# Performance work log

Measured on AMD Instinct MI355X. Metric: run time of the kernel, lower is better.

The kernel has to match this reference:

```python
import jax, jax.numpy as jnp
import numpy as np

N, D, K = 65536, 512, 512


def _l2norm(x, eps=1e-12):
    # matches torch F.normalize: x / max(||x||, eps)
    n = jnp.linalg.norm(x, axis=-1, keepdims=True)
    return x / jnp.maximum(n, eps)


def setup_inputs() -> dict:
    key = jax.random.key(0)
    k1, k2 = jax.random.split(key)
    return {
        "embeddings": jax.random.normal(k1, (N, D), dtype=jnp.float32),
        "labels": jax.random.randint(k2, (N,), 0, K),
        "w": jnp.asarray(10.0, dtype=jnp.float32),
        "b": jnp.asarray(-5.0, dtype=jnp.float32),
        "num_classes": K,
    }


def reference(embeddings, labels, w, b, num_classes):
    # assumes labels take all values in [0, num_classes) so torch.unique's
    # inverse == labels (holds for the generated inputs: 65536 draws over 512 ids)
    labels = labels.astype(jnp.int32)
    n = embeddings.shape[0]
    emb = _l2norm(embeddings)                                        # [N, D]
    ones = jnp.ones((n,), dtype=emb.dtype)
    counts = jax.ops.segment_sum(ones, labels, num_segments=num_classes)   # [K]
    sums = jax.ops.segment_sum(emb, labels, num_segments=num_classes)      # [K, D]
    centroids = sums / jnp.maximum(counts, 1.0)[:, None]             # [K, D] (NOT re-normalized, per source)
    sims = emb @ centroids.T                                          # [N, K]
    # exclusive centroid for each sample's own class, vectorized over N
    cnt_i = counts[labels]                                            # [N]
    denom = jnp.maximum(cnt_i - 1.0, 1.0)[:, None]
    excl = _l2norm((sums[labels] - emb) / denom)                      # [N, D]
    own = jnp.sum(emb * excl, axis=-1)                                # [N]
    rows = jnp.arange(n)
    cur = sims[rows, labels]
    own = jnp.where(cnt_i > 1.0, own, cur)                            # skip singleton classes
    sims = sims.at[rows, labels].set(own)
    logits = jnp.maximum(w, 1e-6) * sims + b
    logp = jax.nn.log_softmax(logits, axis=-1)
    return -jnp.mean(logp[rows, labels])
```

## Files before the change

kernel.cpp:

```cpp
#include <hip/hip_runtime.h>
#include <hip/hip_bf16.h>

#define N_ROWS 65536
#define DIM    512
#define KCLS   512
#define BUCKET 256

typedef __bf16 bf16x8 __attribute__((ext_vector_type(8)));
typedef float  f32x16 __attribute__((ext_vector_type(16)));

__device__ __forceinline__ float bf2f(ushort u) {
    union { unsigned int i; float f; } v; v.i = ((unsigned int)u) << 16; return v.f;
}

__global__ __launch_bounds__(256) void rnorm_embb_kernel(
    const float* __restrict__ emb, const int* __restrict__ labels,
    ushort* __restrict__ embb, int* __restrict__ counts,
    ushort* __restrict__ order16)
{
    const int tid  = threadIdx.x;
    const int wave = tid >> 6;
    const int lane = tid & 63;
    const int row  = blockIdx.x * 4 + wave;

    const float4* ep = (const float4*)(emb + (size_t)row * DIM + lane * 8);
    const float4 e0 = ep[0], e1 = ep[1];
    float ss = e0.x*e0.x + e0.y*e0.y + e0.z*e0.z + e0.w*e0.w
             + e1.x*e1.x + e1.y*e1.y + e1.z*e1.z + e1.w*e1.w;
    #pragma unroll
    for (int off = 1; off < 64; off <<= 1)
        ss += __shfl_xor(ss, off, 64);
    const float rn = 1.0f / fmaxf(sqrtf(ss), 1e-12f);

    bf16x8 h;
    h[0] = (__bf16)(e0.x * rn); h[1] = (__bf16)(e0.y * rn);
    h[2] = (__bf16)(e0.z * rn); h[3] = (__bf16)(e0.w * rn);
    h[4] = (__bf16)(e1.x * rn); h[5] = (__bf16)(e1.y * rn);
    h[6] = (__bf16)(e1.z * rn); h[7] = (__bf16)(e1.w * rn);
    *(bf16x8*)(embb + (size_t)row * DIM + lane * 8) = h;

    if (lane == 0) {
        const int l   = labels[row];
        const int pos = atomicAdd(&counts[l], 1);
        order16[l * BUCKET + pos] = (ushort)row;
    }
}

__global__ __launch_bounds__(256) void class_sum_kernel(
    const ushort* __restrict__ embb,
    const int* __restrict__ counts, const ushort* __restrict__ order16,
    float* __restrict__ sums, ushort* __restrict__ centb)
{
    __shared__ float part[4][DIM];

    const int cls  = blockIdx.x;
    const int tid  = threadIdx.x;
    const int wave = tid >> 6;
    const int lane = tid & 63;
    const int cnt  = counts[cls];
    const int base = cls * BUCKET;
    const int d8   = lane * 8;

    float a[8] = {};
    float b2[8] = {};
    int j = wave;
    for (; j + 4 < cnt; j += 8) {
        const int r1 = order16[base + j];
        const int r2 = order16[base + j + 4];
        const uint4 u1 = *(const uint4*)(embb + (size_t)r1 * DIM + d8);
        const uint4 u2 = *(const uint4*)(embb + (size_t)r2 * DIM + d8);
        const ushort* s1 = (const ushort*)&u1;
        const ushort* s2 = (const ushort*)&u2;
        #pragma unroll
        for (int q = 0; q < 8; ++q) { a[q] += bf2f(s1[q]); b2[q] += bf2f(s2[q]); }
    }
    if (j < cnt) {
        const int r = order16[base + j];
        const uint4 u = *(const uint4*)(embb + (size_t)r * DIM + d8);
        const ushort* s1 = (const ushort*)&u;
        #pragma unroll
        for (int q = 0; q < 8; ++q) a[q] += bf2f(s1[q]);
    }
    #pragma unroll
    for (int q = 0; q < 8; ++q) part[wave][d8 + q] = a[q] + b2[q];
    __syncthreads();

    const int d0 = tid * 2;
    const float s0 = part[0][d0]   + part[1][d0]   + part[2][d0]   + part[3][d0];
    const float s1 = part[0][d0+1] + part[1][d0+1] + part[2][d0+1] + part[3][d0+1];
    *(float2*)(sums + (size_t)cls * DIM + d0) = make_float2(s0, s1);
    const float cinv = 1.0f / fmaxf((float)cnt, 1.0f);
    const __bf16 c0 = (__bf16)(s0 * cinv);
    const __bf16 c1 = (__bf16)(s1 * cinv);
    ushort2 cpk;
    cpk.x = *(const ushort*)&c0;
    cpk.y = *(const ushort*)&c1;
    *(ushort2*)(centb + (size_t)cls * DIM + d0) = cpk;
}

#define A_STRIDE 40
#define B_STRIDE 40
__global__ __launch_bounds__(256, 3) void fused_loss_kernel(
    const ushort* __restrict__ embb, const int* __restrict__ labels,
    const int* __restrict__ counts, const float* __restrict__ sums,
    const ushort* __restrict__ centb,
    const float* __restrict__ wp, const float* __restrict__ bp,
    float* __restrict__ loss_acc, int* __restrict__ done,
    float* __restrict__ out)
{
    __shared__ __align__(16) ushort A_lds[64 * A_STRIDE];
    __shared__ __align__(16) ushort B_lds[256 * B_STRIDE];
    __shared__ float m_part[4][64];
    __shared__ float s_part[4][64];
    __shared__ float ll_s[64];
    __shared__ float own_s[64];
    __shared__ int   lbl_s[64];
    __shared__ int   rep_s[64];

    const int tid  = threadIdx.x;
    const int wave = tid >> 6;
    const int lane = tid & 63;
    const int ln31 = lane & 31;
    const int half = lane >> 5;
    const int r0   = blockIdx.x * 64;

    m_part[wave][lane] = -1e30f;
    s_part[wave][lane] = 0.f;

    for (int rr = wave; rr < 64; rr += 4) {
        const int row = r0 + rr;
        const int l   = labels[row];
        const uint4 ev = *(const uint4*)(embb + (size_t)row * DIM + lane * 8);
        const ushort* eu = (const ushort*)&ev;
        const float4* sp = (const float4*)(sums + (size_t)l * DIM + lane * 8);
        const float4 s0 = sp[0], s1 = sp[1];
        const float sv[8] = {s0.x, s0.y, s0.z, s0.w, s1.x, s1.y, s1.z, s1.w};
        float d1 = 0.f, d2 = 0.f;
        #pragma unroll
        for (int jj = 0; jj < 8; ++jj) {
            const float e  = bf2f(eu[jj]);
            const float df = sv[jj] - e;
            d1 += e * df;
            d2 += df * df;
        }
        #pragma unroll
        for (int off = 32; off > 0; off >>= 1) {
            d1 += __shfl_down(d1, off, 64);
            d2 += __shfl_down(d2, off, 64);
        }
        if (lane == 0) {
            own_s[rr] = d1 / fmaxf(sqrtf(d2), 1e-12f);
            lbl_s[rr] = l;
            rep_s[rr] = (counts[l] > 1) ? 1 : 0;
        }
    }
    __syncthreads();

    const int srow = tid >> 2;
    const int sch  = (tid & 3) * 8;
    const ushort* aSrc = embb + (size_t)(r0 + srow) * DIM + sch;
    ushort* aDst = A_lds + srow * A_STRIDE + sch;
    ushort* bDst = B_lds + srow * B_STRIDE + sch;
    const ushort* Ard = A_lds + ln31 * A_STRIDE + half * 8;
    const ushort* Brd = B_lds + (wave * 64 + ln31) * B_STRIDE + half * 8;

    const int rot = (blockIdx.x * 7) & 15;
    const float wv = fmaxf(wp[0], 1e-6f);
    const float bv = bp[0];

    #pragma unroll 1
    for (int ph = 0; ph < 2; ++ph) {
        const ushort* bBase = centb + (size_t)(ph * 256) * DIM;
        f32x16 acc[2][2] = {};

        #pragma unroll 1
        for (int ic = 0; ic < 16; ++ic) {
            const int kk = ((ic + rot) & 15) * 32;
            *(uint4*)aDst = *(const uint4*)(aSrc + kk);
            #pragma unroll
            for (int it = 0; it < 4; ++it)
                *(uint4*)(bDst + it * 64 * B_STRIDE) =
                    *(const uint4*)(bBase + (size_t)(srow + it * 64) * DIM + sch + kk);
            __syncthreads();

            #pragma unroll
            for (int ks = 0; ks < 2; ++ks) {
                const int ko = ks * 16;
                const bf16x8 a0 = *(const bf16x8*)(Ard + ko);
                const bf16x8 a1 = *(const bf16x8*)(Ard + 32 * A_STRIDE + ko);
                const bf16x8 b0 = *(const bf16x8*)(Brd + ko);
                const bf16x8 b1 = *(const bf16x8*)(Brd + 32 * B_STRIDE + ko);
                acc[0][0] = __builtin_amdgcn_mfma_f32_32x32x16_bf16(a0, b0, acc[0][0], 0, 0, 0);
                acc[0][1] = __builtin_amdgcn_mfma_f32_32x32x16_bf16(a0, b1, acc[0][1], 0, 0, 0);
                acc[1][0] = __builtin_amdgcn_mfma_f32_32x32x16_bf16(a1, b0, acc[1][0], 0, 0, 0);
                acc[1][1] = __builtin_amdgcn_mfma_f32_32x32x16_bf16(a1, b1, acc[1][1], 0, 0, 0);
            }
            __syncthreads();
        }

        #pragma unroll
        for (int mt = 0; mt < 2; ++mt) {
            #pragma unroll
            for (int reg = 0; reg < 16; ++reg) {
                const int row = mt * 32 + (reg & 3) + 8 * (reg >> 2) + 4 * half;
                const int lbl = lbl_s[row];
                float vals[2];
                float mx = -1e30f;
                #pragma unroll
                for (int jn = 0; jn < 2; ++jn) {
                    const int col = ph * 256 + wave * 64 + jn * 32 + ln31;
                    float lg = wv * acc[mt][jn][reg] + bv;
                    if (col == lbl) {
                        if (rep_s[row]) lg = wv * own_s[row] + bv;
                        ll_s[row] = lg;
                    }
                    vals[jn] = lg;
                    mx = fmaxf(mx, lg);
                }
                #pragma unroll
                for (int off = 1; off < 32; off <<= 1)
                    mx = fmaxf(mx, __shfl_xor(mx, off, 64));
                float s = __expf(vals[0] - mx) + __expf(vals[1] - mx);
                #pragma unroll
                for (int off = 1; off < 32; off <<= 1)
                    s += __shfl_xor(s, off, 64);
                if (ln31 == 0) {
                    const float mo = m_part[wave][row];
                    const float mn = fmaxf(mo, mx);
                    s_part[wave][row] = s_part[wave][row] * __expf(mo - mn)
                                      + s * __expf(mx - mn);
                    m_part[wave][row] = mn;
                }
            }
        }
    }
    __syncthreads();

    if (tid < 64) {
        const int row = tid;
        float m0 = m_part[0][row], m1 = m_part[1][row];
        float m2 = m_part[2][row], m3 = m_part[3][row];
        float mt = fmaxf(fmaxf(m0, m1), fmaxf(m2, m3));
        float st = s_part[0][row] * __expf(m0 - mt)
                 + s_part[1][row] * __expf(m1 - mt)
                 + s_part[2][row] * __expf(m2 - mt)
                 + s_part[3][row] * __expf(m3 - mt);
        float loss = mt + __logf(st) - ll_s[row];
        #pragma unroll
        for (int off = 32; off > 0; off >>= 1)
            loss += __shfl_down(loss, off, 64);
        if (tid == 0) {
            atomicAdd(loss_acc, loss);
            __threadfence();
            const int t = atomicAdd(done, 1);
            if (t == (N_ROWS / 64) - 1) {
                const float tot = atomicAdd(loss_acc, 0.0f);
                out[0] = tot / (float)N_ROWS;
            }
        }
    }
}

extern "C" void kernel_launch(void* const* d_in, const int* in_sizes, int n_in,
                              void* d_out, int out_size, void* d_ws, size_t ws_size,
                              hipStream_t stream)
{
    const float* emb    = (const float*)d_in[0];
    const int*   labels = (const int*)d_in[1];
    const float* wp     = (const float*)d_in[2];
    const float* bp     = (const float*)d_in[3];
    float* out = (float*)d_out;

    char* ws = (char*)d_ws;
    ushort* embb    = (ushort*)(ws + 0);
    ushort* order16 = (ushort*)(ws + 67108864);
    float*  sums    = (float*) (ws + 67371008);
    ushort* centb   = (ushort*)(ws + 68419584);
    int*    counts  = (int*)   (ws + 68943872);
    float*  loss_acc= (float*) (ws + 68945920);
    int*    done    = (int*)   (ws + 68945924);

    hipMemsetAsync(counts, 0, 2056, stream);

    rnorm_embb_kernel<<<N_ROWS / 4, 256, 0, stream>>>(emb, labels, embb, counts, order16);
    class_sum_kernel<<<KCLS, 256, 0, stream>>>(embb, counts, order16, sums, centb);
    fused_loss_kernel<<<N_ROWS / 64, 256, 0, stream>>>(embb, labels, counts, sums,
                                                       centb, wp, bp, loss_acc, done, out);
}
```

Before: 331.4 us.

## Retile fused loss GEMM to 128 rows, 8 waves, register-streamed centroids

The fused loss kernel moves from 64-row blocks of 4 waves, which made two passes over 256-class halves, to 128-row blocks of 8 waves that each own 64 classes and cover all 512 in a single pass. Centroid fragments are now read straight from global memory into registers instead of being staged through LDS. The embedding tile is double-buffered in LDS, with the next K-slice prefetched while MFMAs run on the current one. The aim is to cut LDS traffic and barriers and to overlap loads with compute, at the cost of more accumulator registers (launch bounds 512,2) and uncoalesced global reads for the B operand.

```diff
diff --git a/kernel.cpp b/kernel.cpp
--- a/kernel.cpp
+++ b/kernel.cpp
@@ -98,9 +98,26 @@
     *(ushort2*)(centb + (size_t)cls * DIM + d0) = cpk;
 }
 
-#define A_STRIDE 40
-#define B_STRIDE 40
-__global__ __launch_bounds__(256, 3) void fused_loss_kernel(
+#define BM    128
+#define BK    32
+#define A_ST  40
+#define ABUF  (BM * A_ST)
+
+#define MFMA_BK(AR_, B0_, B1_)                                                          \
+    { const bf16x8 a0_ = *(const bf16x8*)((AR_));                                       \
+      const bf16x8 a1_ = *(const bf16x8*)((AR_) + 32 * A_ST);                           \
+      const bf16x8 a2_ = *(const bf16x8*)((AR_) + 64 * A_ST);                           \
+      const bf16x8 a3_ = *(const bf16x8*)((AR_) + 96 * A_ST);                           \
+      acc[0][0] = __builtin_amdgcn_mfma_f32_32x32x16_bf16(a0_, B0_, acc[0][0], 0,0,0);  \
+      acc[1][0] = __builtin_amdgcn_mfma_f32_32x32x16_bf16(a1_, B0_, acc[1][0], 0,0,0);  \
+      acc[2][0] = __builtin_amdgcn_mfma_f32_32x32x16_bf16(a2_, B0_, acc[2][0], 0,0,0);  \
+      acc[3][0] = __builtin_amdgcn_mfma_f32_32x32x16_bf16(a3_, B0_, acc[3][0], 0,0,0);  \
+      acc[0][1] = __builtin_amdgcn_mfma_f32_32x32x16_bf16(a0_, B1_, acc[0][1], 0,0,0);  \
+      acc[1][1] = __builtin_amdgcn_mfma_f32_32x32x16_bf16(a1_, B1_, acc[1][1], 0,0,0);  \
+      acc[2][1] = __builtin_amdgcn_mfma_f32_32x32x16_bf16(a2_, B1_, acc[2][1], 0,0,0);  \
+      acc[3][1] = __builtin_amdgcn_mfma_f32_32x32x16_bf16(a3_, B1_, acc[3][1], 0,0,0); }
+
+__global__ __launch_bounds__(512, 2) void fused_loss_kernel(
     const ushort* __restrict__ embb, const int* __restrict__ labels,
     const int* __restrict__ counts, const float* __restrict__ sums,
     const ushort* __restrict__ centb,
@@ -108,26 +125,22 @@
     float* __restrict__ loss_acc, int* __restrict__ done,
     float* __restrict__ out)
 {
-    __shared__ __align__(16) ushort A_lds[64 * A_STRIDE];
-    __shared__ __align__(16) ushort B_lds[256 * B_STRIDE];
-    __shared__ float m_part[4][64];
-    __shared__ float s_part[4][64];
-    __shared__ float ll_s[64];
-    __shared__ float own_s[64];
-    __shared__ int   lbl_s[64];
-    __shared__ int   rep_s[64];
+    __shared__ __align__(16) ushort A_lds[2 * ABUF];
+    __shared__ float m_ws[8][BM];
+    __shared__ float s_ws[8][BM];
+    __shared__ float ll_s[BM];
+    __shared__ float own_s[BM];
+    __shared__ int   lbl_s[BM];
+    __shared__ int   rep_s[BM];
 
     const int tid  = threadIdx.x;
-    const int wave = tid >> 6;
+    const int wid  = tid >> 6;
     const int lane = tid & 63;
     const int ln31 = lane & 31;
     const int half = lane >> 5;
-    const int r0   = blockIdx.x * 64;
-
-    m_part[wave][lane] = -1e30f;
-    s_part[wave][lane] = 0.f;
-
-    for (int rr = wave; rr < 64; rr += 4) {
+    const int r0   = blockIdx.x * BM;
+
+    for (int rr = wid; rr < BM; rr += 8) {
         const int row = r0 + rr;
         const int l   = labels[row];
         const uint4 ev = *(const uint4*)(embb + (size_t)row * DIM + lane * 8);
@@ -154,106 +167,117 @@
             rep_s[rr] = (counts[l] > 1) ? 1 : 0;
         }
     }
-    __syncthreads();
-
-    const int srow = tid >> 2;
-    const int sch  = (tid & 3) * 8;
-    const ushort* aSrc = embb + (size_t)(r0 + srow) * DIM + sch;
-    ushort* aDst = A_lds + srow * A_STRIDE + sch;
-    ushort* bDst = B_lds + srow * B_STRIDE + sch;
-    const ushort* Ard = A_lds + ln31 * A_STRIDE + half * 8;
-    const ushort* Brd = B_lds + (wave * 64 + ln31) * B_STRIDE + half * 8;
-
-    const int rot = (blockIdx.x * 7) & 15;
+
+    const int rowS = tid >> 2;
+    const int offS = (tid & 3) * 8;
+    const ushort* aSrc = embb + (size_t)(r0 + rowS) * DIM + offS;
+    ushort* aDst = A_lds + rowS * A_ST + offS;
+
+    const int cb = wid * 64;
+    const ushort* bP0 = centb + (size_t)(cb + ln31) * DIM + half * 8;
+    const ushort* bP1 = bP0 + (size_t)32 * DIM;
+    const ushort* aRd = A_lds + ln31 * A_ST + half * 8;
+
     const float wv = fmaxf(wp[0], 1e-6f);
     const float bv = bp[0];
 
+    f32x16 acc[4][2] = {};
+
+    uint4  aE = *(const uint4*)aSrc;
+    bf16x8 bE00 = *(const bf16x8*)(bP0);
+    bf16x8 bE01 = *(const bf16x8*)(bP0 + 16);
+    bf16x8 bE10 = *(const bf16x8*)(bP1);
+    bf16x8 bE11 = *(const bf16x8*)(bP1 + 16);
+    uint4  aO;
+    bf16x8 bO00, bO01, bO10, bO11;
+    *(uint4*)aDst = aE;
+    __syncthreads();
+
     #pragma unroll 1
-    for (int ph = 0; ph < 2; ++ph) {
-        const ushort* bBase = centb + (size_t)(ph * 256) * DIM;
-        f32x16 acc[2][2] = {};
-
-        #pragma unroll 1
-        for (int ic = 0; ic < 16; ++ic) {
-            const int kk = ((ic + rot) & 15) * 32;
-            *(uint4*)aDst = *(const uint4*)(aSrc + kk);
+    for (int d = 0; d < 8; ++d) {
+        const int t0 = 2 * d;
+        {
+            const int tn = t0 + 1;
+            aO   = *(const uint4*) (aSrc + tn * BK);
+            bO00 = *(const bf16x8*)(bP0 + tn * BK);
+            bO01 = *(const bf16x8*)(bP0 + tn * BK + 16);
+            bO10 = *(const bf16x8*)(bP1 + tn * BK);
+            bO11 = *(const bf16x8*)(bP1 + tn * BK + 16);
+            const ushort* ar_ = aRd;
+            MFMA_BK(ar_,      bE00, bE10);
+            MFMA_BK(ar_ + 16, bE01, bE11);
+            *(uint4*)(aDst + ABUF) = aO;
+            __syncthreads();
+        }
+        {
+            const int tn = t0 + 2;
+            if (tn < 16) {
+                aE   = *(const uint4*) (aSrc + tn * BK);
+                bE00 = *(const bf16x8*)(bP0 + tn * BK);
+                bE01 = *(const bf16x8*)(bP0 + tn * BK + 16);
+                bE10 = *(const bf16x8*)(bP1 + tn * BK);
+                bE11 = *(const bf16x8*)(bP1 + tn * BK + 16);
+            }
+            const ushort* ar_ = aRd + ABUF;
+            MFMA_BK(ar_,      bO00, bO10);
+            MFMA_BK(ar_ + 16, bO01, bO11);
+            if (tn < 16) {
+                *(uint4*)aDst = aE;
+                __syncthreads();
+            }
+        }
+    }
+
+    #pragma unroll
+    for (int mt = 0; mt < 4; ++mt) {
+        #pragma unroll
+        for (int reg = 0; reg < 16; ++reg) {
+            const int row = mt * 32 + (reg & 3) + 8 * (reg >> 2) + 4 * half;
+            float v0 = wv * acc[mt][0][reg] + bv;
+            float v1 = wv * acc[mt][1][reg] + bv;
+            const int lbl = lbl_s[row];
+            const int c0  = cb + ln31;
+            if (c0 == lbl) {
+                if (rep_s[row]) v0 = wv * own_s[row] + bv;
+                ll_s[row] = v0;
+            }
+            if (c0 + 32 == lbl) {
+                if (rep_s[row]) v1 = wv * own_s[row] + bv;
+                ll_s[row] = v1;
+            }
+            float mx = fmaxf(v0, v1);
             #pragma unroll
-            for (int it = 0; it < 4; ++it)
-                *(uint4*)(bDst + it * 64 * B_STRIDE) =
-                    *(const uint4*)(bBase + (size_t)(srow + it * 64) * DIM + sch + kk);
-            __syncthreads();
-
+            for (int off = 1; off < 32; off <<= 1)
+                mx = fmaxf(mx, __shfl_xor(mx, off, 64));
+            float s = __expf(v0 - mx) + __expf(v1 - mx);
             #pragma unroll
-            for (int ks = 0; ks < 2; ++ks) {
-                const int ko = ks * 16;
-                const bf16x8 a0 = *(const bf16x8*)(Ard + ko);
-                const bf16x8 a1 = *(const bf16x8*)(Ard + 32 * A_STRIDE + ko);
-                const bf16x8 b0 = *(const bf16x8*)(Brd + ko);
-                const bf16x8 b1 = *(const bf16x8*)(Brd + 32 * B_STRIDE + ko);
-                acc[0][0] = __builtin_amdgcn_mfma_f32_32x32x16_bf16(a0, b0, acc[0][0], 0, 0, 0);
-                acc[0][1] = __builtin_amdgcn_mfma_f32_32x32x16_bf16(a0, b1, acc[0][1], 0, 0, 0);
-                acc[1][0] = __builtin_amdgcn_mfma_f32_32x32x16_bf16(a1, b0, acc[1][0], 0, 0, 0);
-                acc[1][1] = __builtin_amdgcn_mfma_f32_32x32x16_bf16(a1, b1, acc[1][1], 0, 0, 0);
-            }
-            __syncthreads();
-        }
-
-        #pragma unroll
-        for (int mt = 0; mt < 2; ++mt) {
+            for (int off = 1; off < 32; off <<= 1)
+                s += __shfl_xor(s, off, 64);
+            if (ln31 == 0) { m_ws[wid][row] = mx; s_ws[wid][row] = s; }
+        }
+    }
+    __syncthreads();
+
+    if (tid < 64) {
+        float lsum = 0.f;
+        #pragma unroll
+        for (int rr = tid; rr < BM; rr += 64) {
+            float m = m_ws[0][rr];
             #pragma unroll
-            for (int reg = 0; reg < 16; ++reg) {
-                const int row = mt * 32 + (reg & 3) + 8 * (reg >> 2) + 4 * half;
-                const int lbl = lbl_s[row];
-                float vals[2];
-                float mx = -1e30f;
-                #pragma unroll
-                for (int jn = 0; jn < 2; ++jn) {
-                    const int col = ph * 256 + wave * 64 + jn * 32 + ln31;
-                    float lg = wv * acc[mt][jn][reg] + bv;
-                    if (col == lbl) {
-                        if (rep_s[row]) lg = wv * own_s[row] + bv;
-                        ll_s[row] = lg;
-                    }
-                    vals[jn] = lg;
-                    mx = fmaxf(mx, lg);
-                }
-                #pragma unroll
-                for (int off = 1; off < 32; off <<= 1)
-                    mx = fmaxf(mx, __shfl_xor(mx, off, 64));
-                float s = __expf(vals[0] - mx) + __expf(vals[1] - mx);
-                #pragma unroll
-                for (int off = 1; off < 32; off <<= 1)
-                    s += __shfl_xor(s, off, 64);
-                if (ln31 == 0) {
-                    const float mo = m_part[wave][row];
-                    const float mn = fmaxf(mo, mx);
-                    s_part[wave][row] = s_part[wave][row] * __expf(mo - mn)
-                                      + s * __expf(mx - mn);
-                    m_part[wave][row] = mn;
-                }
-            }
-        }
-    }
-    __syncthreads();
-
-    if (tid < 64) {
-        const int row = tid;
-        float m0 = m_part[0][row], m1 = m_part[1][row];
-        float m2 = m_part[2][row], m3 = m_part[3][row];
-        float mt = fmaxf(fmaxf(m0, m1), fmaxf(m2, m3));
-        float st = s_part[0][row] * __expf(m0 - mt)
-                 + s_part[1][row] * __expf(m1 - mt)
-                 + s_part[2][row] * __expf(m2 - mt)
-                 + s_part[3][row] * __expf(m3 - mt);
-        float loss = mt + __logf(st) - ll_s[row];
+            for (int w = 1; w < 8; ++w) m = fmaxf(m, m_ws[w][rr]);
+            float s = 0.f;
+            #pragma unroll
+            for (int w = 0; w < 8; ++w) s += s_ws[w][rr] * __expf(m_ws[w][rr] - m);
+            lsum += m + __logf(s) - ll_s[rr];
+        }
         #pragma unroll
         for (int off = 32; off > 0; off >>= 1)
-            loss += __shfl_down(loss, off, 64);
+            lsum += __shfl_down(lsum, off, 64);
         if (tid == 0) {
-            atomicAdd(loss_acc, loss);
+            atomicAdd(loss_acc, lsum);
             __threadfence();
             const int t = atomicAdd(done, 1);
-            if (t == (N_ROWS / 64) - 1) {
+            if (t == (N_ROWS / BM) - 1) {
                 const float tot = atomicAdd(loss_acc, 0.0f);
                 out[0] = tot / (float)N_ROWS;
             }
@@ -284,6 +308,6 @@
 
     rnorm_embb_kernel<<<N_ROWS / 4, 256, 0, stream>>>(emb, labels, embb, counts, order16);
     class_sum_kernel<<<KCLS, 256, 0, stream>>>(embb, counts, order16, sums, centb);
-    fused_loss_kernel<<<N_ROWS / 64, 256, 0, stream>>>(embb, labels, counts, sums,
+    fused_loss_kernel<<<N_ROWS / BM, 512, 0, stream>>>(embb, labels, counts, sums,
                                                        centb, wp, bp, loss_acc, done, out);
 }
```

Measured after the change: 362.7 us. 9.5% more time.

## Replace LDS-staged GEMM with direct global-to-register MFMA operand loads

Applied to the files above, without the earlier changes.

The fused loss kernel no longer stages embedding and centroid tiles through LDS with per-chunk barriers. Each wave now loads its MFMA operands straight from global memory (centroids via nontemporal loads) and covers 128 classes in a single pass over K, so the two-phase online-softmax merge goes away. The aim is to remove LDS traffic and the barrier stalls. In exchange it relies on L2/L1 for reuse of the A rows across the 4 waves and of the centroids across blocks, uses more accumulator registers (launch bounds drop to 2 blocks), and issues uncoalesced 16-byte loads strided by row.

```diff
diff --git a/kernel.cpp b/kernel.cpp
--- a/kernel.cpp
+++ b/kernel.cpp
@@ -98,9 +98,11 @@
     *(ushort2*)(centb + (size_t)cls * DIM + d0) = cpk;
 }
 
-#define A_STRIDE 40
-#define B_STRIDE 40
-__global__ __launch_bounds__(256, 3) void fused_loss_kernel(
+#define BM 64
+
+#define MFMA(d_, a_, b_) d_ = __builtin_amdgcn_mfma_f32_32x32x16_bf16(a_, b_, d_, 0, 0, 0)
+
+__global__ __launch_bounds__(256, 2) void fused_loss_kernel(
     const ushort* __restrict__ embb, const int* __restrict__ labels,
     const int* __restrict__ counts, const float* __restrict__ sums,
     const ushort* __restrict__ centb,
@@ -108,26 +110,21 @@
     float* __restrict__ loss_acc, int* __restrict__ done,
     float* __restrict__ out)
 {
-    __shared__ __align__(16) ushort A_lds[64 * A_STRIDE];
-    __shared__ __align__(16) ushort B_lds[256 * B_STRIDE];
-    __shared__ float m_part[4][64];
-    __shared__ float s_part[4][64];
-    __shared__ float ll_s[64];
-    __shared__ float own_s[64];
-    __shared__ int   lbl_s[64];
-    __shared__ int   rep_s[64];
+    __shared__ float m_ws[4][BM];
+    __shared__ float s_ws[4][BM];
+    __shared__ float ll_s[BM];
+    __shared__ float own_s[BM];
+    __shared__ int   lbl_s[BM];
+    __shared__ int   rep_s[BM];
 
     const int tid  = threadIdx.x;
-    const int wave = tid >> 6;
+    const int wid  = tid >> 6;
     const int lane = tid & 63;
     const int ln31 = lane & 31;
     const int half = lane >> 5;
-    const int r0   = blockIdx.x * 64;
-
-    m_part[wave][lane] = -1e30f;
-    s_part[wave][lane] = 0.f;
-
-    for (int rr = wave; rr < 64; rr += 4) {
+    const int r0   = blockIdx.x * BM;
+
+    for (int rr = wid; rr < BM; rr += 4) {
         const int row = r0 + rr;
         const int l   = labels[row];
         const uint4 ev = *(const uint4*)(embb + (size_t)row * DIM + lane * 8);
@@ -156,96 +153,83 @@
     }
     __syncthreads();
 
-    const int srow = tid >> 2;
-    const int sch  = (tid & 3) * 8;
-    const ushort* aSrc = embb + (size_t)(r0 + srow) * DIM + sch;
-    ushort* aDst = A_lds + srow * A_STRIDE + sch;
-    ushort* bDst = B_lds + srow * B_STRIDE + sch;
-    const ushort* Ard = A_lds + ln31 * A_STRIDE + half * 8;
-    const ushort* Brd = B_lds + (wave * 64 + ln31) * B_STRIDE + half * 8;
-
-    const int rot = (blockIdx.x * 7) & 15;
+    const int cb = wid * 128;
+    const ushort* aB0 = embb  + (size_t)(r0 + ln31) * DIM + half * 8;
+    const ushort* aB1 = aB0 + (size_t)32 * DIM;
+    const ushort* bB0 = centb + (size_t)(cb + ln31) * DIM + half * 8;
+    const ushort* bB1 = bB0 + (size_t)32 * DIM;
+    const ushort* bB2 = bB0 + (size_t)64 * DIM;
+    const ushort* bB3 = bB0 + (size_t)96 * DIM;
+
     const float wv = fmaxf(wp[0], 1e-6f);
     const float bv = bp[0];
 
-    #pragma unroll 1
-    for (int ph = 0; ph < 2; ++ph) {
-        const ushort* bBase = centb + (size_t)(ph * 256) * DIM;
-        f32x16 acc[2][2] = {};
-
-        #pragma unroll 1
-        for (int ic = 0; ic < 16; ++ic) {
-            const int kk = ((ic + rot) & 15) * 32;
-            *(uint4*)aDst = *(const uint4*)(aSrc + kk);
+    f32x16 acc[2][4] = {};
+
+    #pragma unroll 2
+    for (int t = 0; t < 16; ++t) {
+        const int ko = t * 32;
+        const bf16x8 a00 = *(const bf16x8*)(aB0 + ko);
+        const bf16x8 a10 = *(const bf16x8*)(aB1 + ko);
+        const bf16x8 a01 = *(const bf16x8*)(aB0 + ko + 16);
+        const bf16x8 a11 = *(const bf16x8*)(aB1 + ko + 16);
+        const bf16x8 b00 = __builtin_nontemporal_load((const bf16x8*)(bB0 + ko));
+        const bf16x8 b10 = __builtin_nontemporal_load((const bf16x8*)(bB1 + ko));
+        const bf16x8 b20 = __builtin_nontemporal_load((const bf16x8*)(bB2 + ko));
+        const bf16x8 b30 = __builtin_nontemporal_load((const bf16x8*)(bB3 + ko));
+        const bf16x8 b01 = __builtin_nontemporal_load((const bf16x8*)(bB0 + ko + 16));
+        const bf16x8 b11 = __builtin_nontemporal_load((const bf16x8*)(bB1 + ko + 16));
+        const bf16x8 b21 = __builtin_nontemporal_load((const bf16x8*)(bB2 + ko + 16));
+        const bf16x8 b31 = __builtin_nontemporal_load((const bf16x8*)(bB3 + ko + 16));
+
+        MFMA(acc[0][0], a00, b00); MFMA(acc[1][0], a10, b00);
+        MFMA(acc[0][1], a00, b10); MFMA(acc[1][1], a10, b10);
+        MFMA(acc[0][2], a00, b20); MFMA(acc[1][2], a10, b20);
+        MFMA(acc[0][3], a00, b30); MFMA(acc[1][3], a10, b30);
+        MFMA(acc[0][0], a01, b01); MFMA(acc[1][0], a11, b01);
+        MFMA(acc[0][1], a01, b11); MFMA(acc[1][1], a11, b11);
+        MFMA(acc[0][2], a01, b21); MFMA(acc[1][2], a11, b21);
+        MFMA(acc[0][3], a01, b31); MFMA(acc[1][3], a11, b31);
+    }
+
+    #pragma unroll
+    for (int mt = 0; mt < 2; ++mt) {
+        #pragma unroll
+        for (int reg = 0; reg < 16; ++reg) {
+            const int row = mt * 32 + (reg & 3) + 8 * (reg >> 2) + 4 * half;
+            const int lbl = lbl_s[row];
+            float v0 = wv * acc[mt][0][reg] + bv;
+            float v1 = wv * acc[mt][1][reg] + bv;
+            float v2 = wv * acc[mt][2][reg] + bv;
+            float v3 = wv * acc[mt][3][reg] + bv;
+            const int c = cb + ln31;
+            if (c == lbl)      { if (rep_s[row]) v0 = wv * own_s[row] + bv; ll_s[row] = v0; }
+            if (c + 32 == lbl) { if (rep_s[row]) v1 = wv * own_s[row] + bv; ll_s[row] = v1; }
+            if (c + 64 == lbl) { if (rep_s[row]) v2 = wv * own_s[row] + bv; ll_s[row] = v2; }
+            if (c + 96 == lbl) { if (rep_s[row]) v3 = wv * own_s[row] + bv; ll_s[row] = v3; }
+            float mx = fmaxf(fmaxf(v0, v1), fmaxf(v2, v3));
             #pragma unroll
-            for (int it = 0; it < 4; ++it)
-                *(uint4*)(bDst + it * 64 * B_STRIDE) =
-                    *(const uint4*)(bBase + (size_t)(srow + it * 64) * DIM + sch + kk);
-            __syncthreads();
-
+            for (int off = 1; off < 32; off <<= 1)
+                mx = fmaxf(mx, __shfl_xor(mx, off, 64));
+            float s = __expf(v0 - mx) + __expf(v1 - mx)
+                    + __expf(v2 - mx) + __expf(v3 - mx);
             #pragma unroll
-            for (int ks = 0; ks < 2; ++ks) {
-                const int ko = ks * 16;
-                const bf16x8 a0 = *(const bf16x8*)(Ard + ko);
-                const bf16x8 a1 = *(const bf16x8*)(Ard + 32 * A_STRIDE + ko);
-                const bf16x8 b0 = *(const bf16x8*)(Brd + ko);
-                const bf16x8 b1 = *(const bf16x8*)(Brd + 32 * B_STRIDE + ko);
-                acc[0][0] = __builtin_amdgcn_mfma_f32_32x32x16_bf16(a0, b0, acc[0][0], 0, 0, 0);
-                acc[0][1] = __builtin_amdgcn_mfma_f32_32x32x16_bf16(a0, b1, acc[0][1], 0, 0, 0);
-                acc[1][0] = __builtin_amdgcn_mfma_f32_32x32x16_bf16(a1, b0, acc[1][0], 0, 0, 0);
-                acc[1][1] = __builtin_amdgcn_mfma_f32_32x32x16_bf16(a1, b1, acc[1][1], 0, 0, 0);
-            }
-            __syncthreads();
-        }
-
-        #pragma unroll
-        for (int mt = 0; mt < 2; ++mt) {
-            #pragma unroll
-            for (int reg = 0; reg < 16; ++reg) {
-                const int row = mt * 32 + (reg & 3) + 8 * (reg >> 2) + 4 * half;
-                const int lbl = lbl_s[row];
-                float vals[2];
-                float mx = -1e30f;
-                #pragma unroll
-                for (int jn = 0; jn < 2; ++jn) {
-                    const int col = ph * 256 + wave * 64 + jn * 32 + ln31;
-                    float lg = wv * acc[mt][jn][reg] + bv;
-                    if (col == lbl) {
-                        if (rep_s[row]) lg = wv * own_s[row] + bv;
-                        ll_s[row] = lg;
-                    }
-                    vals[jn] = lg;
-                    mx = fmaxf(mx, lg);
-                }
-                #pragma unroll
-                for (int off = 1; off < 32; off <<= 1)
-                    mx = fmaxf(mx, __shfl_xor(mx, off, 64));
-                float s = __expf(vals[0] - mx) + __expf(vals[1] - mx);
-                #pragma unroll
-                for (int off = 1; off < 32; off <<= 1)
-                    s += __shfl_xor(s, off, 64);
-                if (ln31 == 0) {
-                    const float mo = m_part[wave][row];
-                    const float mn = fmaxf(mo, mx);
-                    s_part[wave][row] = s_part[wave][row] * __expf(mo - mn)
-                                      + s * __expf(mx - mn);
-                    m_part[wave][row] = mn;
-                }
-            }
+            for (int off = 1; off < 32; off <<= 1)
+                s += __shfl_xor(s, off, 64);
+            if (ln31 == 0) { m_ws[wid][row] = mx; s_ws[wid][row] = s; }
         }
     }
     __syncthreads();
 
     if (tid < 64) {
-        const int row = tid;
-        float m0 = m_part[0][row], m1 = m_part[1][row];
-        float m2 = m_part[2][row], m3 = m_part[3][row];
-        float mt = fmaxf(fmaxf(m0, m1), fmaxf(m2, m3));
-        float st = s_part[0][row] * __expf(m0 - mt)
-                 + s_part[1][row] * __expf(m1 - mt)
-                 + s_part[2][row] * __expf(m2 - mt)
-                 + s_part[3][row] * __expf(m3 - mt);
-        float loss = mt + __logf(st) - ll_s[row];
+        const int rr = tid;
+        float m = m_ws[0][rr];
+        #pragma unroll
+        for (int w = 1; w < 4; ++w) m = fmaxf(m, m_ws[w][rr]);
+        float s = 0.f;
+        #pragma unroll
+        for (int w = 0; w < 4; ++w) s += s_ws[w][rr] * __expf(m_ws[w][rr] - m);
+        float loss = m + __logf(s) - ll_s[rr];
         #pragma unroll
         for (int off = 32; off > 0; off >>= 1)
             loss += __shfl_down(loss, off, 64);
@@ -253,7 +237,7 @@
             atomicAdd(loss_acc, loss);
             __threadfence();
             const int t = atomicAdd(done, 1);
-            if (t == (N_ROWS / 64) - 1) {
+            if (t == (N_ROWS / BM) - 1) {
                 const float tot = atomicAdd(loss_acc, 0.0f);
                 out[0] = tot / (float)N_ROWS;
             }
@@ -284,6 +268,6 @@
 
     rnorm_embb_kernel<<<N_ROWS / 4, 256, 0, stream>>>(emb, labels, embb, counts, order16);
     class_sum_kernel<<<KCLS, 256, 0, stream>>>(embb, counts, order16, sums, centb);
-    fused_loss_kernel<<<N_ROWS / 64, 256, 0, stream>>>(embb, labels, counts, sums,
+    fused_loss_kernel<<<N_ROWS / BM, 256, 0, stream>>>(embb, labels, counts, sums,
                                                        centb, wp, bp, loss_acc, done, out);
 }
```

Measured after the change: 416.4 us. 1.26x slower.
